# Kernel optimization log

Measured on AMD Instinct MI355X. Metric: run time of the kernel, lower is better.

Reference implementation:

```python
import jax, jax.numpy as jnp
import numpy as np

SCALING = 2.0  # lora_alpha / r = 32 / 16


def setup_inputs() -> dict:
    key = jax.random.key(0)
    ks = jax.random.split(key, 5)
    N, D, E, R = 8192, 4096, 8, 16
    x = jax.random.normal(ks[0], (N, D), dtype=jnp.float32)
    base_W = jax.random.normal(ks[1], (D, D), dtype=jnp.float32) * (1.0 / np.sqrt(D))
    gate_W = jax.random.normal(ks[2], (E, D), dtype=jnp.float32) * (1.0 / np.sqrt(D))
    A = jax.random.normal(ks[3], (E, R, D), dtype=jnp.float32) * 0.01
    B = jax.random.normal(ks[4], (D, R), dtype=jnp.float32)[None] * jnp.ones((E, 1, 1)) * 0.01
    return {"x": x, "base_W": base_W, "gate_W": gate_W, "A": A, "B": B, "top_k": 2}


def reference(x, base_W, gate_W, A, B, top_k):
    N, D = x.shape
    E = gate_W.shape[0]
    # base linear (torch Linear: y = x @ W.T)
    result = x @ base_W.T
    # gate: top-k logits, softmax over the k selected (in fp32, cast back)
    gate_logits = x @ gate_W.T                      # [N, E]
    top_vals, top_idx = jax.lax.top_k(gate_logits, top_k)  # [N, k]
    w = jax.nn.softmax(top_vals.astype(jnp.float32), axis=-1).astype(x.dtype)
    # dense per-token per-expert routing weight (0 if not selected)
    w_full = jnp.zeros((N, E), dtype=x.dtype).at[
        jnp.arange(N)[:, None], top_idx].add(w)    # [N, E]
    # all-expert LoRA (matches the original dense loop over experts)
    ax = jnp.einsum('nd,erd->ner', x, A)            # [N, E, r]
    bx = jnp.einsum('ner,eor->neo', ax, B)          # [N, E, D]
    result = result + SCALING * jnp.einsum('neo,ne->no', bx, w_full)
    return result
```

## Files before the change

### kernel.cpp

```cpp
#include <hip/hip_runtime.h>
#include <math.h>


#define NTOK 8192
#define DIM  4096
#define NEXP 8
#define RANK 16
#define KAUG (NEXP * RANK)
#define KSPLIT 4

typedef __bf16 bf16x8 __attribute__((ext_vector_type(8)));
typedef float  f32x4  __attribute__((ext_vector_type(4)));

__device__ __forceinline__ unsigned short f2bf(float f) {
    union { float f; unsigned int u; } v;
    v.f = f;
    unsigned int u = v.u;
    return (unsigned short)((u + 0x7fffu + ((u >> 16) & 1u)) >> 16);
}

__global__ __launch_bounds__(256) void k_cvt(
    const float4* __restrict__ in, ushort4* __restrict__ outv, int n4)
{
    int i = blockIdx.x * 256 + threadIdx.x;
    if (i < n4) {
        float4 v = in[i];
        outv[i] = make_ushort4(f2bf(v.x), f2bf(v.y), f2bf(v.z), f2bf(v.w));
    }
}

__global__ __launch_bounds__(256) void k_bt(
    const float* __restrict__ B, unsigned short* __restrict__ Bt)
{
    int idx = blockIdx.x * 256 + threadIdx.x;
    int o = idx >> 7;
    int j = idx & 127;
    int e = j >> 4;
    int r = j & 15;
    Bt[idx] = f2bf(B[((size_t)e * DIM + o) * RANK + r]);
}

__global__ __launch_bounds__(256) void k_gate(
    const float* __restrict__ x,
    const float* __restrict__ gW,
    float4* __restrict__ gate_out,
    ushort4* __restrict__ xb4)
{
    __shared__ float xs[DIM];
    __shared__ float logits[NEXP];
    const int n = blockIdx.x;

    const float4* xr = (const float4*)(x + (size_t)n * DIM);
    ushort4* xw = xb4 + (size_t)n * (DIM / 4);
    for (int c = threadIdx.x; c < DIM / 4; c += 256) {
        float4 v = xr[c];
        xs[4 * c + 0] = v.x;
        xs[4 * c + 1] = v.y;
        xs[4 * c + 2] = v.z;
        xs[4 * c + 3] = v.w;
        xw[c] = make_ushort4(f2bf(v.x), f2bf(v.y), f2bf(v.z), f2bf(v.w));
    }
    __syncthreads();

    const int wave = threadIdx.x >> 6;
    const int lane = threadIdx.x & 63;
    for (int e = wave; e < NEXP; e += 4) {
        const float* g = gW + (size_t)e * DIM;
        float s = 0.f;
        for (int i = lane; i < DIM; i += 64) s += xs[i] * g[i];
        #pragma unroll
        for (int off = 32; off; off >>= 1) s += __shfl_down(s, off);
        if (lane == 0) logits[e] = s;
    }
    __syncthreads();

    if (threadIdx.x == 0) {
        int e0 = 0; float v0 = logits[0];
        #pragma unroll
        for (int e = 1; e < NEXP; ++e)
            if (logits[e] > v0) { v0 = logits[e]; e0 = e; }
        int e1 = -1; float v1 = -INFINITY;
        #pragma unroll
        for (int e = 0; e < NEXP; ++e)
            if (e != e0 && logits[e] > v1) { v1 = logits[e]; e1 = e; }
        float b = __expf(v1 - v0);
        float w0 = 1.f / (1.f + b);
        float w1 = 1.f - w0;
        gate_out[n] = make_float4((float)e0, (float)e1, w0, w1);
    }
}

__device__ __forceinline__ void stage_lds(
    const unsigned short* gbase, int strideElems,
    unsigned short* ldsBase, int wave, int lane)
{
    const int l8 = lane >> 3;
    const int c8 = ((lane & 7) ^ l8) << 3;
    #pragma unroll
    for (int q = 0; q < 4; ++q) {
        const int r = wave * 32 + q * 8;
        const unsigned short* gp = gbase + (size_t)(r + l8) * strideElems + c8;
        unsigned short* lp = ldsBase + r * 64;
        __builtin_amdgcn_global_load_lds(
            (const __attribute__((address_space(1))) void*)gp,
            (__attribute__((address_space(3))) void*)lp,
            16, 0, 0);
    }
}

__device__ __forceinline__ void mfma_step(
    const unsigned short* As, const unsigned short* Bs,
    int waveM, int waveN, int lane, f32x4 acc[4][4])
{
    const int quad = lane >> 4;
    const int l15  = lane & 15;
    const int x7   = l15 & 7;
    #pragma unroll
    for (int s = 0; s < 2; ++s) {
        const int chunk = (s << 2) | quad;
        const int po = ((chunk ^ x7) << 3);
        bf16x8 af[4], bfv[4];
        #pragma unroll
        for (int i = 0; i < 4; ++i)
            af[i] = *(const bf16x8*)(As + (waveM * 64 + i * 16 + l15) * 64 + po);
        #pragma unroll
        for (int j = 0; j < 4; ++j)
            bfv[j] = *(const bf16x8*)(Bs + (waveN * 64 + j * 16 + l15) * 64 + po);
        #pragma unroll
        for (int i = 0; i < 4; ++i)
            #pragma unroll
            for (int j = 0; j < 4; ++j)
                acc[i][j] = __builtin_amdgcn_mfma_f32_16x16x32_bf16(
                    af[i], bfv[j], acc[i][j], 0, 0, 0);
    }
}

__global__ __launch_bounds__(256) void k_ax(
    const unsigned short* __restrict__ xb,
    const unsigned short* __restrict__ Ab,
    float* __restrict__ axPart)
{
    __shared__ __align__(16) unsigned short As[128 * 64];
    __shared__ __align__(16) unsigned short Bs[128 * 64];
    const int tid  = threadIdx.x;
    const int wave = tid >> 6, lane = tid & 63;
    const int waveM = wave >> 1, waveN = wave & 1;
    const int rowBase = blockIdx.x * 128;
    const int ks = blockIdx.y;
    const int k0 = ks * (DIM / KSPLIT);

    f32x4 acc[4][4] = {};

    for (int it = 0; it < (DIM / KSPLIT) / 64; ++it) {
        stage_lds(xb + (size_t)rowBase * DIM + k0 + it * 64, DIM, As, wave, lane);
        stage_lds(Ab + (size_t)0 * DIM       + k0 + it * 64, DIM, Bs, wave, lane);
        __syncthreads();
        mfma_step(As, Bs, waveM, waveN, lane, acc);
        __syncthreads();
    }

    float* outp = axPart + (size_t)ks * NTOK * KAUG;
    const int quad = lane >> 4, l15 = lane & 15;
    #pragma unroll
    for (int i = 0; i < 4; ++i) {
        #pragma unroll
        for (int j = 0; j < 4; ++j) {
            const int gc = waveN * 64 + j * 16 + l15;
            #pragma unroll
            for (int t = 0; t < 4; ++t) {
                const int gr = rowBase + waveM * 64 + i * 16 + quad * 4 + t;
                outp[(size_t)gr * KAUG + gc] = acc[i][j][t];
            }
        }
    }
}

__global__ __launch_bounds__(256) void k_scale(
    const float* __restrict__ axPart,
    const float4* __restrict__ gate_out,
    unsigned short* __restrict__ cB)
{
    int idx = blockIdx.x * 256 + threadIdx.x;
    int n = idx >> 7;
    int j = idx & 127;
    float s = 0.f;
    #pragma unroll
    for (int ks = 0; ks < KSPLIT; ++ks)
        s += axPart[(size_t)ks * NTOK * KAUG + idx];
    float4 g = gate_out[n];
    int e  = j >> 4;
    int e0 = (int)g.x;
    int e1 = (int)g.y;
    float scale = (e == e0) ? 2.f * g.z : (e == e1) ? 2.f * g.w : 0.f;
    cB[idx] = f2bf(scale * s);
}

__global__ __launch_bounds__(256) void k_main(
    const unsigned short* __restrict__ xb,
    const unsigned short* __restrict__ Wb,
    const unsigned short* __restrict__ cB,
    const unsigned short* __restrict__ Bt,
    float* __restrict__ out)
{
    __shared__ __align__(16) unsigned short As[128 * 64];
    __shared__ __align__(16) unsigned short Bs[128 * 64];
    const int tid  = threadIdx.x;
    const int wave = tid >> 6, lane = tid & 63;
    const int waveM = wave >> 1, waveN = wave & 1;
    const int rowBase = blockIdx.y * 128;
    const int colBase = blockIdx.x * 128;

    f32x4 acc[4][4] = {};

    for (int it = 0; it < DIM / 64; ++it) {
        stage_lds(xb + (size_t)rowBase * DIM + it * 64, DIM, As, wave, lane);
        stage_lds(Wb + (size_t)colBase * DIM + it * 64, DIM, Bs, wave, lane);
        __syncthreads();
        mfma_step(As, Bs, waveM, waveN, lane, acc);
        __syncthreads();
    }
    for (int it = 0; it < KAUG / 64; ++it) {
        stage_lds(cB + (size_t)rowBase * KAUG + it * 64, KAUG, As, wave, lane);
        stage_lds(Bt + (size_t)colBase * KAUG + it * 64, KAUG, Bs, wave, lane);
        __syncthreads();
        mfma_step(As, Bs, waveM, waveN, lane, acc);
        __syncthreads();
    }

    const int quad = lane >> 4, l15 = lane & 15;
    #pragma unroll
    for (int i = 0; i < 4; ++i) {
        #pragma unroll
        for (int j = 0; j < 4; ++j) {
            const int gc = colBase + waveN * 64 + j * 16 + l15;
            #pragma unroll
            for (int t = 0; t < 4; ++t) {
                const int gr = rowBase + waveM * 64 + i * 16 + quad * 4 + t;
                out[(size_t)gr * DIM + gc] = acc[i][j][t];
            }
        }
    }
}

extern "C" void kernel_launch(void* const* d_in, const int* in_sizes, int n_in,
                              void* d_out, int out_size, void* d_ws, size_t ws_size,
                              hipStream_t stream) {
    (void)in_sizes; (void)n_in; (void)out_size; (void)ws_size;

    const float* x  = (const float*)d_in[0];
    const float* bW = (const float*)d_in[1];
    const float* gW = (const float*)d_in[2];
    const float* A  = (const float*)d_in[3];
    const float* B  = (const float*)d_in[4];
    float* out = (float*)d_out;

    char* ws = (char*)d_ws;
    float4*         gate_out = (float4*)ws;
    unsigned short* xb = (unsigned short*)(ws + (1u << 17));
    unsigned short* Wb = xb + (size_t)NTOK * DIM;
    unsigned short* Ab = Wb + (size_t)DIM * DIM;
    unsigned short* Bt = Ab + (size_t)KAUG * DIM;
    unsigned short* cB = Bt + (size_t)DIM * KAUG;
    float*      axPart = (float*)(cB + (size_t)NTOK * KAUG);

    k_gate<<<NTOK, 256, 0, stream>>>(x, gW, gate_out, (ushort4*)xb);
    k_cvt <<<(DIM * DIM / 4 + 255) / 256, 256, 0, stream>>>(
        (const float4*)bW, (ushort4*)Wb, DIM * DIM / 4);
    k_cvt <<<(KAUG * DIM / 4 + 255) / 256, 256, 0, stream>>>(
        (const float4*)A, (ushort4*)Ab, KAUG * DIM / 4);
    k_bt  <<<(DIM * KAUG) / 256, 256, 0, stream>>>(B, Bt);
    k_ax  <<<dim3(NTOK / 128, KSPLIT), 256, 0, stream>>>(xb, Ab, axPart);
    k_scale<<<(NTOK * KAUG) / 256, 256, 0, stream>>>(axPart, gate_out, cB);
    k_main<<<dim3(DIM / 128, NTOK / 128), 256, 0, stream>>>(xb, Wb, cB, Bt, out);
}
```

Before: 719.3 us.

## Rewrite main GEMM with 256x256 tiles, double-buffered async LDS loads, swizzle

Replaces the simple 128x128 synchronous-staging GEMM with a 512-thread, 256x256-tile kernel. Global-to-LDS copies are issued directly into a double buffer and overlapped with MFMA compute. LDS reads are XOR-swizzled to avoid bank conflicts, and block IDs are remapped for L2 locality. The main and LoRA K-loops are merged into one pipelined loop. The cost is 128KB of LDS and heavy register use, which limits occupancy, and the hand-written waitcnt and barrier scheduling is fragile.

```diff
diff --git a/kernel.cpp b/kernel.cpp
--- a/kernel.cpp
+++ b/kernel.cpp
@@ -8,6 +8,7 @@
 #define RANK 16
 #define KAUG (NEXP * RANK)
 #define KSPLIT 4
+#define NKT  ((DIM + KAUG) / 64)
 
 typedef __bf16 bf16x8 __attribute__((ext_vector_type(8)));
 typedef float  f32x4  __attribute__((ext_vector_type(4)));
@@ -195,48 +196,126 @@
     cB[idx] = f2bf(scale * s);
 }
 
-__global__ __launch_bounds__(256) void k_main(
+__global__ __launch_bounds__(512) void k_main(
     const unsigned short* __restrict__ xb,
     const unsigned short* __restrict__ Wb,
     const unsigned short* __restrict__ cB,
     const unsigned short* __restrict__ Bt,
     float* __restrict__ out)
 {
-    __shared__ __align__(16) unsigned short As[128 * 64];
-    __shared__ __align__(16) unsigned short Bs[128 * 64];
+    __shared__ __align__(16) unsigned short sA[2][256 * 64];
+    __shared__ __align__(16) unsigned short sB[2][256 * 64];
+
     const int tid  = threadIdx.x;
     const int wave = tid >> 6, lane = tid & 63;
-    const int waveM = wave >> 1, waveN = wave & 1;
-    const int rowBase = blockIdx.y * 128;
-    const int colBase = blockIdx.x * 128;
-
-    f32x4 acc[4][4] = {};
-
-    for (int it = 0; it < DIM / 64; ++it) {
-        stage_lds(xb + (size_t)rowBase * DIM + it * 64, DIM, As, wave, lane);
-        stage_lds(Wb + (size_t)colBase * DIM + it * 64, DIM, Bs, wave, lane);
-        __syncthreads();
-        mfma_step(As, Bs, waveM, waveN, lane, acc);
-        __syncthreads();
-    }
-    for (int it = 0; it < KAUG / 64; ++it) {
-        stage_lds(cB + (size_t)rowBase * KAUG + it * 64, KAUG, As, wave, lane);
-        stage_lds(Bt + (size_t)colBase * KAUG + it * 64, KAUG, Bs, wave, lane);
-        __syncthreads();
-        mfma_step(As, Bs, waveM, waveN, lane, acc);
-        __syncthreads();
-    }
-
+    const int wm = wave >> 2, wn = wave & 3;
     const int quad = lane >> 4, l15 = lane & 15;
-    #pragma unroll
-    for (int i = 0; i < 4; ++i) {
-        #pragma unroll
-        for (int j = 0; j < 4; ++j) {
-            const int gc = colBase + waveN * 64 + j * 16 + l15;
+    const int x7 = l15 & 7;
+
+    const int bid = blockIdx.x;
+    const int swz = (bid & 7) * 64 + (bid >> 3);
+    const int rowBase = (swz >> 4) * 256;
+    const int colBase = (swz & 15) * 256;
+
+    const unsigned short* aMain = xb + (size_t)rowBase * DIM;
+    const unsigned short* bMain = Wb + (size_t)colBase * DIM;
+    const unsigned short* aLora = cB + (size_t)rowBase * KAUG;
+    const unsigned short* bLora = Bt + (size_t)colBase * KAUG;
+
+    const int l8 = lane >> 3;
+    const int c8 = ((lane & 7) ^ l8) << 3;
+
+    auto stageT = [&](int t, int half, bool isA) {
+        if (t >= NKT) return;
+        unsigned short* ldsR = isA ? &sA[t & 1][0] : &sB[t & 1][0];
+        const unsigned short* g;
+        int stride;
+        if (t < DIM / 64) { g = (isA ? aMain : bMain) + t * 64;              stride = DIM;  }
+        else              { g = (isA ? aLora : bLora) + (t - DIM / 64) * 64; stride = KAUG; }
+        #pragma unroll
+        for (int qq = 0; qq < 2; ++qq) {
+            const int r0 = half * 128 + qq * 64 + wave * 8;
+            const unsigned short* gp = g + (size_t)(r0 + l8) * stride + c8;
+            unsigned short* lp = ldsR + r0 * 64;
+            __builtin_amdgcn_global_load_lds(
+                (const __attribute__((address_space(1))) void*)gp,
+                (__attribute__((address_space(3))) void*)lp,
+                16, 0, 0);
+        }
+    };
+
+    f32x4 acc[8][4] = {};
+
+    stageT(0, 0, true);  stageT(0, 1, true);
+    stageT(0, 0, false); stageT(0, 1, false);
+    stageT(1, 0, false); stageT(1, 1, false);
+    asm volatile("s_waitcnt vmcnt(4)" ::: "memory");
+    __builtin_amdgcn_s_barrier();
+
+    #pragma unroll 2
+    for (int k = 0; k < NKT; ++k) {
+        const unsigned short* At = &sA[k & 1][0];
+        const unsigned short* Bl = &sB[k & 1][0];
+        bf16x8 bFr[4][2];
+        #pragma unroll
+        for (int q = 0; q < 4; ++q) {
+            bf16x8 aFr[2][2];
+            #pragma unroll
+            for (int mi = 0; mi < 2; ++mi)
+                #pragma unroll
+                for (int ksl = 0; ksl < 2; ++ksl) {
+                    const int r  = wm * 128 + (q * 2 + mi) * 16 + l15;
+                    const int ch = ksl * 4 + quad;
+                    aFr[mi][ksl] = *(const bf16x8*)(At + r * 64 + ((ch ^ x7) << 3));
+                }
+            if (q == 0) {
+                #pragma unroll
+                for (int nf = 0; nf < 4; ++nf)
+                    #pragma unroll
+                    for (int ksl = 0; ksl < 2; ++ksl) {
+                        const int r  = wn * 64 + nf * 16 + l15;
+                        const int ch = ksl * 4 + quad;
+                        bFr[nf][ksl] = *(const bf16x8*)(Bl + r * 64 + ((ch ^ x7) << 3));
+                    }
+            }
+            if      (q == 0) stageT(k + 1, 0, true);
+            else if (q == 1) stageT(k + 1, 1, true);
+            else if (q == 2) stageT(k + 2, 0, false);
+            else             stageT(k + 2, 1, false);
+
+            __builtin_amdgcn_s_barrier();
+            asm volatile("s_waitcnt lgkmcnt(0)" ::: "memory");
+            __builtin_amdgcn_sched_barrier(0);
+            __builtin_amdgcn_s_setprio(1);
+            #pragma unroll
+            for (int mi = 0; mi < 2; ++mi)
+                #pragma unroll
+                for (int nf = 0; nf < 4; ++nf)
+                    #pragma unroll
+                    for (int ksl = 0; ksl < 2; ++ksl)
+                        acc[q * 2 + mi][nf] = __builtin_amdgcn_mfma_f32_16x16x32_bf16(
+                            aFr[mi][ksl], bFr[nf][ksl], acc[q * 2 + mi][nf], 0, 0, 0);
+            __builtin_amdgcn_s_setprio(0);
+            __builtin_amdgcn_sched_barrier(0);
+            if (q == 3) {
+                if (k == NKT - 2)
+                    asm volatile("s_waitcnt vmcnt(0)" ::: "memory");
+                else if (k < NKT - 2)
+                    asm volatile("s_waitcnt vmcnt(4)" ::: "memory");
+            }
+            __builtin_amdgcn_s_barrier();
+        }
+    }
+
+    #pragma unroll
+    for (int mf = 0; mf < 8; ++mf) {
+        #pragma unroll
+        for (int nf = 0; nf < 4; ++nf) {
+            const int gc = colBase + wn * 64 + nf * 16 + l15;
             #pragma unroll
             for (int t = 0; t < 4; ++t) {
-                const int gr = rowBase + waveM * 64 + i * 16 + quad * 4 + t;
-                out[(size_t)gr * DIM + gc] = acc[i][j][t];
+                const int gr = rowBase + wm * 128 + mf * 16 + quad * 4 + t;
+                out[(size_t)gr * DIM + gc] = acc[mf][nf][t];
             }
         }
     }
@@ -271,5 +350,5 @@
     k_bt  <<<(DIM * KAUG) / 256, 256, 0, stream>>>(B, Bt);
     k_ax  <<<dim3(NTOK / 128, KSPLIT), 256, 0, stream>>>(xb, Ab, axPart);
     k_scale<<<(NTOK * KAUG) / 256, 256, 0, stream>>>(axPart, gate_out, cB);
-    k_main<<<dim3(DIM / 128, NTOK / 128), 256, 0, stream>>>(xb, Wb, cB, Bt, out);
-}
+    k_main<<<dim3(512), dim3(512), 0, stream>>>(xb, Wb, cB, Bt, out);
+}
```

Measured after the change: 691.6 us. 1.04x faster.
